# Kernel optimization log

Hardware: AMD Instinct MI355X
Metric: run time of the kernel (lower is better)

Reference implementation:

```python
import jax, jax.numpy as jnp
import numpy as np

B, S, D = 8, 2048, 1024
NEG = 1e9  # mask penalty used by the original module


def setup_inputs() -> dict:
    key = jax.random.key(0)
    kq, kk, km = jax.random.split(key, 3)
    q = jax.random.normal(kq, (B, S, D), dtype=jnp.float32)
    k = jax.random.normal(kk, (B, S, D), dtype=jnp.float32)
    # True = valid token, False = padding (module uses logical_not(mask) as pad)
    mask = jax.random.randint(km, (B, S), 0, 2).astype(bool)
    # learnable scalar scale, initialized to 1 (use_scale=True)
    scale = jnp.ones((), dtype=jnp.float32)
    return {"q": q, "k": k, "mask": mask, "scale": scale}


def reference(q, k, mask, scale):
    # v = k (sources has 2 entries when mask is provided)
    scores = jnp.einsum("bqd,bkd->bqk", q, k) * scale          # [B,S,S]
    pad = jnp.logical_not(mask).astype(scores.dtype)[:, :, None]  # [B,S,1]
    pad = jnp.maximum(pad, jnp.swapaxes(pad, 1, 2))             # [B,S,S]
    seq = jnp.triu(jnp.ones((S, S), scores.dtype), k=1)[None]   # [1,S,S] causal
    attn_mask = jnp.maximum(pad, seq)
    scores = scores - NEG * attn_mask
    attn = jax.nn.softmax(scores, axis=-1)
    feat = jnp.einsum("bqk,bkd->bqd", attn, k)                  # [B,S,D]
    return feat
```

## Files before the change

kernel.cpp:

```cpp
#include <hip/hip_runtime.h>
#include <hip/hip_bf16.h>
#include <stdint.h>

#define S_ 2048
#define D_ 1024
#define B_ 8
#define KEXP 3072
#define NEGC 1e9f

typedef _Float16 f16;
typedef _Float16 f16x8 __attribute__((ext_vector_type(8)));
typedef float f32x4 __attribute__((ext_vector_type(4)));

#define DSR(dst, addr, off) \
  asm volatile("ds_read_b128 %0, %1 offset:%c2" : "=v"(dst) : "v"(addr), "i"(off))
#define WAITL(n) do { asm volatile("s_waitcnt lgkmcnt(%c0)" :: "i"(n) : "memory"); \
                      __builtin_amdgcn_sched_barrier(0); } while (0)
#define VMC(n) asm volatile("s_waitcnt vmcnt(%c0)" :: "i"(n) : "memory")
#define BAR() __builtin_amdgcn_s_barrier()

__global__ __launch_bounds__(256) void split_expand2(const float* __restrict__ qin,
                                                     const float* __restrict__ kin,
                                                     f16* __restrict__ qx,
                                                     f16* __restrict__ kx) {
  const int isB = blockIdx.y;
  const float* in = isB ? kin : qin;
  f16* out = isB ? kx : qx;
  size_t idx = (size_t)blockIdx.x * 256 + threadIdx.x;
  const float4* ip = (const float4*)(in + idx * 8);
  float4 a = ip[0], b = ip[1];
  float vv[8] = {a.x, a.y, a.z, a.w, b.x, b.y, b.z, b.w};
  union { f16 h[24]; uint4 u[3]; } o;
#pragma unroll
  for (int t = 0; t < 8; ++t) {
    float v = vv[t] * 64.0f;
    f16 h = (f16)v;
    float r = v - (float)h;
    f16 l = (f16)r;
    o.h[3 * t + 0] = h;
    o.h[3 * t + 1] = isB ? h : l;
    o.h[3 * t + 2] = isB ? l : h;
  }
  uint4* op = (uint4*)(out + idx * 24);
  op[0] = o.u[0]; op[1] = o.u[1]; op[2] = o.u[2];
}

__global__ __launch_bounds__(256) void transpose_cast(const float* __restrict__ k,
                                                      f16* __restrict__ khT) {
  __shared__ f16 tile[64][65];
  int j0 = blockIdx.x * 64, d0 = blockIdx.y * 64;
  size_t bz = blockIdx.z;
  const float* kb = k + bz * (size_t)S_ * D_;
  f16* ob = khT + bz * (size_t)D_ * S_;
#pragma unroll
  for (int i = 0; i < 16; ++i) {
    int e = threadIdx.x + i * 256;
    int r = e >> 6, c = e & 63;
    tile[c][r] = (f16)kb[(size_t)(j0 + r) * D_ + d0 + c];
  }
  __syncthreads();
#pragma unroll
  for (int i = 0; i < 16; ++i) {
    int e = threadIdx.x + i * 256;
    int r = e >> 6, c = e & 63;
    ob[(size_t)(d0 + r) * S_ + j0 + c] = tile[r][c];
  }
}

template <int KA, int NN, int BN, int PIPE>
__global__ __launch_bounds__(512, PIPE ? 1 : 2) void gemm8p(const f16* __restrict__ A,
                                                            const f16* __restrict__ Bm,
                                                            float* __restrict__ C,
                                                            const float* scale_ptr,
                                                            float factor) {
  constexpr int NFQ = BN / 128;
  constexpr int GB = NFQ;
  constexpr int NB = 2 * NFQ;
  constexpr int VP3 = 2 + GB;
  constexpr int VP7 = 2 + 2 * GB;
  constexpr int VPR = 4 + 2 * GB;
  constexpr int NI = KA / 128;
  __shared__ f16 AS[2][256 * 64];
  __shared__ f16 BS[2][BN * 64];

  const int tid = threadIdx.x;
  const int lane = tid & 63, wave = tid >> 6;
  const int wm = wave >> 2, wn = wave & 3;
  const int fr = lane & 15, kq = lane >> 4;

  int lin = blockIdx.x + gridDim.x * blockIdx.y;
  int ntot = gridDim.x * gridDim.y;
  int nid = (lin & 7) * (ntot >> 3) + (lin >> 3);
  int bz = nid >> 6, rem = nid & 63;
  int bx = rem & 7, by = rem >> 3;

  const f16* Ab = A + (size_t)bz * S_ * KA + (size_t)bx * 256 * KA;
  const f16* Bb = Bm + (size_t)bz * NN * KA + (size_t)by * BN * KA;

  const int T0 = fr * 128 + (((0 + kq) ^ (fr & 7)) << 4);
  const int T1 = fr * 128 + (((4 + kq) ^ (fr & 7)) << 4);
  uint32_t asbase = (uint32_t)(uintptr_t)(__attribute__((address_space(3))) f16*)&AS[0][0];
  uint32_t bsbase = (uint32_t)(uintptr_t)(__attribute__((address_space(3))) f16*)&BS[0][0];
  uint32_t aA[2][2], aB[2][2];
#pragma unroll
  for (int b = 0; b < 2; ++b) {
    aA[b][0] = asbase + b * 32768 + wm * 8192 + T0;
    aA[b][1] = asbase + b * 32768 + wm * 8192 + T1;
    aB[b][0] = bsbase + b * (BN * 128) + wn * (BN * 16) + T0;
    aB[b][1] = bsbase + b * (BN * 128) + wn * (BN * 16) + T1;
  }

  const int srl = tid >> 3;
  const int sgc = ((((tid * 16) & 127) ^ (((tid >> 3) & 7) << 4)) >> 1);

  auto stgA = [&](int buf, int unit, int kt) {
#pragma unroll
    for (int i = 0; i < 2; ++i) {
      const f16* src = Ab + (size_t)(unit * 128 + i * 64 + srl) * KA + kt * 64 + sgc;
      __builtin_amdgcn_global_load_lds(
          (const __attribute__((address_space(1))) void*)src,
          (__attribute__((address_space(3))) void*)&AS[buf][unit * 8192 + i * 4096 + wave * 512],
          16, 0, 0);
    }
  };
  auto stgB = [&](int buf, int unit, int kt) {
#pragma unroll
    for (int i = 0; i < GB; ++i) {
      const f16* src = Bb + (size_t)(unit * (BN / 2) + i * 64 + srl) * KA + kt * 64 + sgc;
      __builtin_amdgcn_global_load_lds(
          (const __attribute__((address_space(1))) void*)src,
          (__attribute__((address_space(3))) void*)&BS[buf][unit * (BN * 32) + i * 4096 + wave * 512],
          16, 0, 0);
    }
  };

  f32x4 acc[2][2][4][2];
#pragma unroll
  for (int mh = 0; mh < 2; ++mh)
#pragma unroll
    for (int nh = 0; nh < 2; ++nh)
#pragma unroll
      for (int m = 0; m < 4; ++m)
#pragma unroll
        for (int n = 0; n < NFQ; ++n)
#pragma unroll
          for (int r = 0; r < 4; ++r) acc[mh][nh][m][n][r] = 0.0f;

#define ISS_A(DST, UB, MH) do {                  \
    DSR(DST[0], aA[UB][0], (MH)*16384 + 0);      \
    DSR(DST[1], aA[UB][0], (MH)*16384 + 2048);   \
    DSR(DST[2], aA[UB][0], (MH)*16384 + 4096);   \
    DSR(DST[3], aA[UB][0], (MH)*16384 + 6144);   \
    DSR(DST[4], aA[UB][1], (MH)*16384 + 0);      \
    DSR(DST[5], aA[UB][1], (MH)*16384 + 2048);   \
    DSR(DST[6], aA[UB][1], (MH)*16384 + 4096);   \
    DSR(DST[7], aA[UB][1], (MH)*16384 + 6144);   \
  } while (0)

#define ISS_B(DST, UB, NH) do {                       \
    DSR(DST[0], aB[UB][0], (NH) * (BN * 64) + 0);     \
    DSR(DST[1], aB[UB][1], (NH) * (BN * 64) + 0);     \
    if constexpr (NFQ == 2) {                         \
      DSR(DST[2], aB[UB][0], (NH) * (BN * 64) + 2048);\
      DSR(DST[3], aB[UB][1], (NH) * (BN * 64) + 2048);\
    }                                                 \
  } while (0)

#define MMX(MH, NH, AF, BF) do {                                                          \
    __builtin_amdgcn_s_setprio(1);                                                        \
    _Pragma("unroll")                                                                     \
    for (int m = 0; m < 4; ++m) {                                                         \
      acc[MH][NH][m][0] = __builtin_amdgcn_mfma_f32_16x16x32_f16(AF[m], BF[0], acc[MH][NH][m][0], 0, 0, 0);     \
      acc[MH][NH][m][0] = __builtin_amdgcn_mfma_f32_16x16x32_f16(AF[4 + m], BF[1], acc[MH][NH][m][0], 0, 0, 0); \
      if constexpr (NFQ == 2) {                                                           \
        acc[MH][NH][m][1] = __builtin_amdgcn_mfma_f32_16x16x32_f16(AF[m], BF[2], acc[MH][NH][m][1], 0, 0, 0);     \
        acc[MH][NH][m][1] = __builtin_amdgcn_mfma_f32_16x16x32_f16(AF[4 + m], BF[3], acc[MH][NH][m][1], 0, 0, 0); \
      }                                                                                   \
    }                                                                                     \
    __builtin_amdgcn_s_setprio(0);                                                        \
  } while (0)

  if constexpr (!PIPE) {
    stgA(0, 0, 0); stgA(0, 1, 0); stgB(0, 0, 0); stgB(0, 1, 0);
    stgA(1, 0, 1);
    VMC(0); BAR();

#pragma unroll 1
    for (int I = 0; I < NI; ++I) {
      const int v = 2 * I + 1, u2 = 2 * I + 2, v2 = 2 * I + 3;
      const bool st = (I + 1 < NI);
      f16x8 af[8], bf[4];
      ISS_A(af, 0, 0); ISS_B(bf, 0, 0); stgA(1, 1, v);
      WAITL(0); MMX(0, 0, af, bf); BAR();
      ISS_B(bf, 0, 1); stgB(1, 0, v); stgB(1, 1, v);
      WAITL(0); MMX(0, 1, af, bf); BAR();
      ISS_A(af, 0, 1); if (st) stgA(0, 0, u2);
      WAITL(0); MMX(1, 1, af, bf); BAR();
      ISS_B(bf, 0, 0); if (st) stgA(0, 1, u2);
      WAITL(0); MMX(1, 0, af, bf);
      if (st) { VMC(4); } else { VMC(0); }
      BAR();
      ISS_A(af, 1, 0); ISS_B(bf, 1, 0); if (st) stgB(0, 1, u2);
      WAITL(0); MMX(0, 0, af, bf); BAR();
      ISS_B(bf, 1, 1); if (st) stgB(0, 0, u2);
      WAITL(0); MMX(0, 1, af, bf); BAR();
      ISS_A(af, 1, 1); if (st) stgA(1, 0, v2);
      WAITL(0); MMX(1, 1, af, bf); BAR();
      ISS_B(bf, 1, 0);
      WAITL(0); MMX(1, 0, af, bf);
      if (st) { VMC(2); }
      BAR();
    }
  } else {
    f16x8 afX[8], afY[8], bfP[4], bfQ[4];
    stgA(0, 0, 0); stgA(0, 1, 0); stgB(0, 0, 0); stgB(0, 1, 0);
    stgA(1, 0, 1); stgA(1, 1, 1); stgB(1, 0, 1); stgB(1, 1, 1);
    VMC(VPR); BAR();
    ISS_A(afX, 0, 0); ISS_B(bfP, 0, 0);

#pragma unroll 1
    for (int I = 0; I < NI; ++I) {
      const int u2 = 2 * I + 2, v2 = 2 * I + 3;
      const bool st = (I + 1 < NI);
      ISS_B(bfQ, 0, 1);
      WAITL(NB); MMX(0, 0, afX, bfP); BAR();
      ISS_A(afY, 0, 1);
      if (st) stgA(0, 0, u2);
      WAITL(8); MMX(0, 1, afX, bfQ); BAR();
      ISS_B(bfP, 0, 0);
      if (st) stgB(0, 1, u2);
      WAITL(NB); MMX(1, 1, afY, bfQ);
      if (st) { VMC(VP3); } else { VMC(0); }
      BAR();
      ISS_A(afX, 1, 0); ISS_B(bfQ, 1, 0);
      if (st) stgA(0, 1, u2);
      WAITL(8 + NB); MMX(1, 0, afY, bfP); BAR();
      ISS_B(bfP, 1, 1);
      if (st) stgB(0, 0, u2);
      WAITL(NB); MMX(0, 0, afX, bfQ); BAR();
      ISS_A(afY, 1, 1);
      if (st) { stgA(1, 0, v2); stgB(1, 0, v2); }
      WAITL(8); MMX(0, 1, afX, bfP); BAR();
      if (st) stgB(1, 1, v2);
      WAITL(0); MMX(1, 1, afY, bfP);
      if (st) { VMC(VP7); }
      BAR();
      if (st) {
        ISS_A(afX, 0, 0); ISS_B(bfP, 0, 0);
        stgA(1, 1, v2);
        WAITL(8 + NB);
      } else {
        WAITL(0);
      }
      MMX(1, 0, afY, bfQ); BAR();
    }
  }
#undef ISS_A
#undef ISS_B
#undef MMX

  float scl = factor;
  if (scale_ptr != nullptr) scl = factor * scale_ptr[0];
  float* Cb = C + (size_t)bz * S_ * NN;
  const int r0 = bx * 256 + wm * 64 + kq * 4;
  const int c0 = by * BN + wn * (BN / 8) + fr;
#pragma unroll
  for (int mh = 0; mh < 2; ++mh)
#pragma unroll
    for (int nh = 0; nh < 2; ++nh)
#pragma unroll
      for (int m = 0; m < 4; ++m)
#pragma unroll
        for (int n = 0; n < NFQ; ++n)
#pragma unroll
          for (int r = 0; r < 4; ++r)
            Cb[(size_t)(r0 + mh * 128 + m * 16 + r) * NN + c0 + nh * (BN / 2) + n * 16] =
                acc[mh][nh][m][n][r] * scl;
}

__device__ __forceinline__ float block_reduce_max(float v, float* red, int tid) {
#pragma unroll
  for (int o = 32; o > 0; o >>= 1) v = fmaxf(v, __shfl_xor(v, o, 64));
  __syncthreads();
  if ((tid & 63) == 0) red[tid >> 6] = v;
  __syncthreads();
  return fmaxf(fmaxf(red[0], red[1]), fmaxf(red[2], red[3]));
}
__device__ __forceinline__ float block_reduce_sum(float v, float* red, int tid) {
#pragma unroll
  for (int o = 32; o > 0; o >>= 1) v += __shfl_xor(v, o, 64);
  __syncthreads();
  if ((tid & 63) == 0) red[4 + (tid >> 6)] = v;
  __syncthreads();
  return (red[4] + red[5]) + (red[6] + red[7]);
}

__global__ __launch_bounds__(256) void softmax_rows(const float* __restrict__ scores,
                                                    const int* __restrict__ mask,
                                                    const float* __restrict__ qg,
                                                    const float* __restrict__ kg,
                                                    const float* __restrict__ scale_ptr,
                                                    f16* __restrict__ P, int b0) {
  __shared__ float red[8];
  const int q = blockIdx.x, bl = blockIdx.y, bg = b0 + bl;
  const int tid = threadIdx.x;
  const float* srow = scores + ((size_t)bl * S_ + q) * S_;
  f16* prow = P + ((size_t)bl * S_ + q) * S_;
  const int j0 = tid * 8;
  float4 s0v = *(const float4*)(srow + j0);
  float4 s1v = *(const float4*)(srow + j0 + 4);
  float sv[8] = {s0v.x, s0v.y, s0v.z, s0v.w, s1v.x, s1v.y, s1v.z, s1v.w};

  if (mask[bg * S_ + q] == 0) {
    float vv[8];
    float lm = -3.4e38f;
#pragma unroll
    for (int i = 0; i < 8; ++i) {
      vv[i] = sv[i] - NEGC;
      lm = fmaxf(lm, vv[i]);
    }
    float g0 = block_reduce_max(lm, red, tid);
    float lm2 = -3.4e38f;
#pragma unroll 1
    for (int i = 0; i < 8; ++i) {
      float s = sv[i];
      float t = s * (1.0f / 64.0f);
      float rn = rintf(t);
      float dist = (0.5f - fabsf(t - rn)) * 64.0f;
      float v = vv[i];
      if (dist < 1e-3f && v >= g0 - 64.5f) {
        const float* qr = qg + ((size_t)bg * S_ + q) * D_;
        const float* kr = kg + ((size_t)bg * S_ + j0 + i) * D_;
        double acc = 0.0;
        for (int t2 = 0; t2 < D_; ++t2) acc += (double)qr[t2] * (double)kr[t2];
        v = (float)acc * scale_ptr[0] - NEGC;
      }
      vv[i] = v;
      lm2 = fmaxf(lm2, v);
    }
    float gf = block_reduce_max(lm2, red, tid);
    float local = 0.0f;
#pragma unroll
    for (int i = 0; i < 8; ++i) local += (vv[i] == gf) ? 1.0f : 0.0f;
    float cnt = block_reduce_sum(local, red, tid);
    f16 inv = (f16)(1.0f / cnt);
    union { f16 h[8]; uint4 u; } ow;
#pragma unroll
    for (int i = 0; i < 8; ++i) ow.h[i] = (vv[i] == gf) ? inv : (f16)0.0f;
    *(uint4*)(prow + j0) = ow.u;
    return;
  }

  int4 m0 = *(const int4*)(mask + (size_t)bg * S_ + j0);
  int4 m1 = *(const int4*)(mask + (size_t)bg * S_ + j0 + 4);
  int mk[8] = {m0.x, m0.y, m0.z, m0.w, m1.x, m1.y, m1.z, m1.w};
  int fl[8];
  float lm = -3.4e38f;
#pragma unroll
  for (int i = 0; i < 8; ++i) {
    fl[i] = (j0 + i <= q) && (mk[i] != 0);
    if (fl[i]) lm = fmaxf(lm, sv[i]);
  }
  float m = block_reduce_max(lm, red, tid);
  float ls = 0.0f;
#pragma unroll
  for (int i = 0; i < 8; ++i) {
    float e = fl[i] ? expf(sv[i] - m) : 0.0f;
    sv[i] = e; ls += e;
  }
  float sum = block_reduce_sum(ls, red, tid);
  float inv = 1.0f / sum;
  union { f16 h[8]; uint4 u; } ow;
#pragma unroll
  for (int i = 0; i < 8; ++i) ow.h[i] = (f16)(sv[i] * inv);
  *(uint4*)(prow + j0) = ow.u;
}

extern "C" void kernel_launch(void* const* d_in, const int* in_sizes, int n_in,
                              void* d_out, int out_size, void* d_ws, size_t ws_size,
                              hipStream_t stream) {
  (void)in_sizes; (void)n_in; (void)out_size;
  const float* q = (const float*)d_in[0];
  const float* k = (const float*)d_in[1];
  const int* mask = (const int*)d_in[2];
  const float* scale = (const float*)d_in[3];
  float* out = (float*)d_out;

  const size_t per_qx = (size_t)S_ * KEXP * 2;
  const size_t per_khT = (size_t)D_ * S_ * 2;
  const size_t per_sc = (size_t)S_ * S_ * 4;
  const size_t per_batch = 2 * per_qx + per_khT + per_sc;

  int nb = (int)(ws_size / per_batch);
  if (nb > 4) nb = 4;
  if (nb < 1) nb = 1;

  char* w = (char*)d_ws;
  f16* qx = (f16*)w;
  f16* kx = (f16*)(w + (size_t)nb * per_qx);
  f16* khT = (f16*)(w + (size_t)nb * per_qx * 2);
  float* sc = (float*)(w + (size_t)nb * (per_qx * 2 + per_khT));
  f16* P = qx;

  for (int b0 = 0; b0 < B_; b0 += nb) {
    int cb = (B_ - b0 < nb) ? (B_ - b0) : nb;
    const float* qb = q + (size_t)b0 * S_ * D_;
    const float* kb = k + (size_t)b0 * S_ * D_;

    int blocks0 = cb * ((S_ * D_ / 8) / 256);
    split_expand2<<<dim3(blocks0, 2), dim3(256), 0, stream>>>(qb, kb, qx, kx);
    transpose_cast<<<dim3(S_ / 64, D_ / 64, cb), dim3(256), 0, stream>>>(kb, khT);

    gemm8p<KEXP, S_, 256, 0><<<dim3(64, cb), dim3(512), 0, stream>>>(
        qx, kx, sc, scale, 0.000244140625f);

    softmax_rows<<<dim3(S_, cb), dim3(256), 0, stream>>>(sc, mask, q, k, scale, P, b0);

    gemm8p<S_, D_, 128, 1><<<dim3(64, cb), dim3(512), 0, stream>>>(
        P, khT, out + (size_t)b0 * S_ * D_, nullptr, 1.0f);
  }
}
```

Measured before the change: 428.6 us.

## Split GEMM template and give PV GEMM a triple-buffered LDS pipeline

Separates the QK and PV GEMMs into dedicated kernels. The PV GEMM moves to a 3-stage shared-memory ring with 64-wide K steps, issuing global-to-LDS loads two stages ahead and using one barrier per step instead of eight barriers per 128-K iteration. The aim is to cut synchronisation and overlap memory loads with MFMA work. In exchange it uses 1.5x the LDS (144KB) and has coarser waits, which could limit latency hiding within a step.

```diff
diff --git a/kernel.cpp b/kernel.cpp
--- a/kernel.cpp
+++ b/kernel.cpp
@@ -67,18 +67,14 @@
   }
 }
 
-template <int KA, int NN, int BN, int PIPE>
-__global__ __launch_bounds__(512, PIPE ? 1 : 2) void gemm8p(const f16* __restrict__ A,
-                                                            const f16* __restrict__ Bm,
-                                                            float* __restrict__ C,
-                                                            const float* scale_ptr,
-                                                            float factor) {
+template <int KA, int NN, int BN>
+__global__ __launch_bounds__(512, 2) void gemmQK(const f16* __restrict__ A,
+                                                 const f16* __restrict__ Bm,
+                                                 float* __restrict__ C,
+                                                 const float* scale_ptr,
+                                                 float factor) {
   constexpr int NFQ = BN / 128;
   constexpr int GB = NFQ;
-  constexpr int NB = 2 * NFQ;
-  constexpr int VP3 = 2 + GB;
-  constexpr int VP7 = 2 + 2 * GB;
-  constexpr int VPR = 4 + 2 * GB;
   constexpr int NI = KA / 128;
   __shared__ f16 AS[2][256 * 64];
   __shared__ f16 BS[2][BN * 64];
@@ -160,10 +156,8 @@
 #define ISS_B(DST, UB, NH) do {                       \
     DSR(DST[0], aB[UB][0], (NH) * (BN * 64) + 0);     \
     DSR(DST[1], aB[UB][1], (NH) * (BN * 64) + 0);     \
-    if constexpr (NFQ == 2) {                         \
-      DSR(DST[2], aB[UB][0], (NH) * (BN * 64) + 2048);\
-      DSR(DST[3], aB[UB][1], (NH) * (BN * 64) + 2048);\
-    }                                                 \
+    DSR(DST[2], aB[UB][0], (NH) * (BN * 64) + 2048);  \
+    DSR(DST[3], aB[UB][1], (NH) * (BN * 64) + 2048);  \
   } while (0)
 
 #define MMX(MH, NH, AF, BF) do {                                                          \
@@ -172,88 +166,41 @@
     for (int m = 0; m < 4; ++m) {                                                         \
       acc[MH][NH][m][0] = __builtin_amdgcn_mfma_f32_16x16x32_f16(AF[m], BF[0], acc[MH][NH][m][0], 0, 0, 0);     \
       acc[MH][NH][m][0] = __builtin_amdgcn_mfma_f32_16x16x32_f16(AF[4 + m], BF[1], acc[MH][NH][m][0], 0, 0, 0); \
-      if constexpr (NFQ == 2) {                                                           \
-        acc[MH][NH][m][1] = __builtin_amdgcn_mfma_f32_16x16x32_f16(AF[m], BF[2], acc[MH][NH][m][1], 0, 0, 0);     \
-        acc[MH][NH][m][1] = __builtin_amdgcn_mfma_f32_16x16x32_f16(AF[4 + m], BF[3], acc[MH][NH][m][1], 0, 0, 0); \
-      }                                                                                   \
+      acc[MH][NH][m][1] = __builtin_amdgcn_mfma_f32_16x16x32_f16(AF[m], BF[2], acc[MH][NH][m][1], 0, 0, 0);     \
+      acc[MH][NH][m][1] = __builtin_amdgcn_mfma_f32_16x16x32_f16(AF[4 + m], BF[3], acc[MH][NH][m][1], 0, 0, 0); \
     }                                                                                     \
     __builtin_amdgcn_s_setprio(0);                                                        \
   } while (0)
 
-  if constexpr (!PIPE) {
-    stgA(0, 0, 0); stgA(0, 1, 0); stgB(0, 0, 0); stgB(0, 1, 0);
-    stgA(1, 0, 1);
-    VMC(0); BAR();
+  stgA(0, 0, 0); stgA(0, 1, 0); stgB(0, 0, 0); stgB(0, 1, 0);
+  stgA(1, 0, 1);
+  VMC(0); BAR();
 
 #pragma unroll 1
-    for (int I = 0; I < NI; ++I) {
-      const int v = 2 * I + 1, u2 = 2 * I + 2, v2 = 2 * I + 3;
-      const bool st = (I + 1 < NI);
-      f16x8 af[8], bf[4];
-      ISS_A(af, 0, 0); ISS_B(bf, 0, 0); stgA(1, 1, v);
-      WAITL(0); MMX(0, 0, af, bf); BAR();
-      ISS_B(bf, 0, 1); stgB(1, 0, v); stgB(1, 1, v);
-      WAITL(0); MMX(0, 1, af, bf); BAR();
-      ISS_A(af, 0, 1); if (st) stgA(0, 0, u2);
-      WAITL(0); MMX(1, 1, af, bf); BAR();
-      ISS_B(bf, 0, 0); if (st) stgA(0, 1, u2);
-      WAITL(0); MMX(1, 0, af, bf);
-      if (st) { VMC(4); } else { VMC(0); }
-      BAR();
-      ISS_A(af, 1, 0); ISS_B(bf, 1, 0); if (st) stgB(0, 1, u2);
-      WAITL(0); MMX(0, 0, af, bf); BAR();
-      ISS_B(bf, 1, 1); if (st) stgB(0, 0, u2);
-      WAITL(0); MMX(0, 1, af, bf); BAR();
-      ISS_A(af, 1, 1); if (st) stgA(1, 0, v2);
-      WAITL(0); MMX(1, 1, af, bf); BAR();
-      ISS_B(bf, 1, 0);
-      WAITL(0); MMX(1, 0, af, bf);
-      if (st) { VMC(2); }
-      BAR();
-    }
-  } else {
-    f16x8 afX[8], afY[8], bfP[4], bfQ[4];
-    stgA(0, 0, 0); stgA(0, 1, 0); stgB(0, 0, 0); stgB(0, 1, 0);
-    stgA(1, 0, 1); stgA(1, 1, 1); stgB(1, 0, 1); stgB(1, 1, 1);
-    VMC(VPR); BAR();
-    ISS_A(afX, 0, 0); ISS_B(bfP, 0, 0);
-
-#pragma unroll 1
-    for (int I = 0; I < NI; ++I) {
-      const int u2 = 2 * I + 2, v2 = 2 * I + 3;
-      const bool st = (I + 1 < NI);
-      ISS_B(bfQ, 0, 1);
-      WAITL(NB); MMX(0, 0, afX, bfP); BAR();
-      ISS_A(afY, 0, 1);
-      if (st) stgA(0, 0, u2);
-      WAITL(8); MMX(0, 1, afX, bfQ); BAR();
-      ISS_B(bfP, 0, 0);
-      if (st) stgB(0, 1, u2);
-      WAITL(NB); MMX(1, 1, afY, bfQ);
-      if (st) { VMC(VP3); } else { VMC(0); }
-      BAR();
-      ISS_A(afX, 1, 0); ISS_B(bfQ, 1, 0);
-      if (st) stgA(0, 1, u2);
-      WAITL(8 + NB); MMX(1, 0, afY, bfP); BAR();
-      ISS_B(bfP, 1, 1);
-      if (st) stgB(0, 0, u2);
-      WAITL(NB); MMX(0, 0, afX, bfQ); BAR();
-      ISS_A(afY, 1, 1);
-      if (st) { stgA(1, 0, v2); stgB(1, 0, v2); }
-      WAITL(8); MMX(0, 1, afX, bfP); BAR();
-      if (st) stgB(1, 1, v2);
-      WAITL(0); MMX(1, 1, afY, bfP);
-      if (st) { VMC(VP7); }
-      BAR();
-      if (st) {
-        ISS_A(afX, 0, 0); ISS_B(bfP, 0, 0);
-        stgA(1, 1, v2);
-        WAITL(8 + NB);
-      } else {
-        WAITL(0);
-      }
-      MMX(1, 0, afY, bfQ); BAR();
-    }
+  for (int I = 0; I < NI; ++I) {
+    const int v = 2 * I + 1, u2 = 2 * I + 2, v2 = 2 * I + 3;
+    const bool st = (I + 1 < NI);
+    f16x8 af[8], bf[4];
+    ISS_A(af, 0, 0); ISS_B(bf, 0, 0); stgA(1, 1, v);
+    WAITL(0); MMX(0, 0, af, bf); BAR();
+    ISS_B(bf, 0, 1); stgB(1, 0, v); stgB(1, 1, v);
+    WAITL(0); MMX(0, 1, af, bf); BAR();
+    ISS_A(af, 0, 1); if (st) stgA(0, 0, u2);
+    WAITL(0); MMX(1, 1, af, bf); BAR();
+    ISS_B(bf, 0, 0); if (st) stgA(0, 1, u2);
+    WAITL(0); MMX(1, 0, af, bf);
+    if (st) { VMC(4); } else { VMC(0); }
+    BAR();
+    ISS_A(af, 1, 0); ISS_B(bf, 1, 0); if (st) stgB(0, 1, u2);
+    WAITL(0); MMX(0, 0, af, bf); BAR();
+    ISS_B(bf, 1, 1); if (st) stgB(0, 0, u2);
+    WAITL(0); MMX(0, 1, af, bf); BAR();
+    ISS_A(af, 1, 1); if (st) stgA(1, 0, v2);
+    WAITL(0); MMX(1, 1, af, bf); BAR();
+    ISS_B(bf, 1, 0);
+    WAITL(0); MMX(1, 0, af, bf);
+    if (st) { VMC(2); }
+    BAR();
   }
 #undef ISS_A
 #undef ISS_B
@@ -276,6 +223,141 @@
           for (int r = 0; r < 4; ++r)
             Cb[(size_t)(r0 + mh * 128 + m * 16 + r) * NN + c0 + nh * (BN / 2) + n * 16] =
                 acc[mh][nh][m][n][r] * scl;
+}
+
+template <int KA, int NN>
+__global__ __launch_bounds__(512, 1) void gemmPV(const f16* __restrict__ A,
+                                                 const f16* __restrict__ Bm,
+                                                 float* __restrict__ C,
+                                                 float factor) {
+  constexpr int BN = 128;
+  constexpr int NT = KA / 64;
+  __shared__ f16 AS[3][256 * 64];
+  __shared__ f16 BS[3][BN * 64];
+
+  const int tid = threadIdx.x;
+  const int lane = tid & 63, wave = tid >> 6;
+  const int wm = wave >> 2, wn = wave & 3;
+  const int fr = lane & 15, kq = lane >> 4;
+
+  int lin = blockIdx.x + gridDim.x * blockIdx.y;
+  int ntot = gridDim.x * gridDim.y;
+  int nid = (lin & 7) * (ntot >> 3) + (lin >> 3);
+  int bz = nid >> 6, rem = nid & 63;
+  int bx = rem & 7, by = rem >> 3;
+
+  const f16* Ab = A + (size_t)bz * S_ * KA + (size_t)bx * 256 * KA;
+  const f16* Bb = Bm + (size_t)bz * NN * KA + (size_t)by * BN * KA;
+
+  const int T0 = fr * 128 + (((0 + kq) ^ (fr & 7)) << 4);
+  const int T1 = fr * 128 + (((4 + kq) ^ (fr & 7)) << 4);
+  uint32_t asbase = (uint32_t)(uintptr_t)(__attribute__((address_space(3))) f16*)&AS[0][0];
+  uint32_t bsbase = (uint32_t)(uintptr_t)(__attribute__((address_space(3))) f16*)&BS[0][0];
+  uint32_t aA[3][2], aB[3][2];
+#pragma unroll
+  for (int s = 0; s < 3; ++s) {
+    aA[s][0] = asbase + s * 32768 + wm * 8192 + T0;
+    aA[s][1] = asbase + s * 32768 + wm * 8192 + T1;
+    aB[s][0] = bsbase + s * 16384 + wn * (BN * 16) + T0;
+    aB[s][1] = bsbase + s * 16384 + wn * (BN * 16) + T1;
+  }
+
+  const int srl = tid >> 3;
+  const int sgc = ((((tid * 16) & 127) ^ (((tid >> 3) & 7) << 4)) >> 1);
+
+  auto stgA = [&](int slot, int unit, int kt) {
+#pragma unroll
+    for (int i = 0; i < 2; ++i) {
+      const f16* src = Ab + (size_t)(unit * 128 + i * 64 + srl) * KA + kt * 64 + sgc;
+      __builtin_amdgcn_global_load_lds(
+          (const __attribute__((address_space(1))) void*)src,
+          (__attribute__((address_space(3))) void*)&AS[slot][unit * 8192 + i * 4096 + wave * 512],
+          16, 0, 0);
+    }
+  };
+  auto stgB = [&](int slot, int unit, int kt) {
+    const f16* src = Bb + (size_t)(unit * (BN / 2) + srl) * KA + kt * 64 + sgc;
+    __builtin_amdgcn_global_load_lds(
+        (const __attribute__((address_space(1))) void*)src,
+        (__attribute__((address_space(3))) void*)&BS[slot][unit * (BN * 32) + wave * 512],
+        16, 0, 0);
+  };
+
+  f32x4 acc[2][2][4];
+#pragma unroll
+  for (int mh = 0; mh < 2; ++mh)
+#pragma unroll
+    for (int nh = 0; nh < 2; ++nh)
+#pragma unroll
+      for (int m = 0; m < 4; ++m)
+#pragma unroll
+        for (int r = 0; r < 4; ++r) acc[mh][nh][m][r] = 0.0f;
+
+#define PISS_A(DST, S, MH) do {                  \
+    DSR(DST[0], aA[S][0], (MH)*16384 + 0);       \
+    DSR(DST[1], aA[S][0], (MH)*16384 + 2048);    \
+    DSR(DST[2], aA[S][0], (MH)*16384 + 4096);    \
+    DSR(DST[3], aA[S][0], (MH)*16384 + 6144);    \
+    DSR(DST[4], aA[S][1], (MH)*16384 + 0);       \
+    DSR(DST[5], aA[S][1], (MH)*16384 + 2048);    \
+    DSR(DST[6], aA[S][1], (MH)*16384 + 4096);    \
+    DSR(DST[7], aA[S][1], (MH)*16384 + 6144);    \
+  } while (0)
+
+#define PISS_B(DST, S, NH) do {                       \
+    DSR(DST[0], aB[S][0], (NH) * (BN * 64) + 0);      \
+    DSR(DST[1], aB[S][1], (NH) * (BN * 64) + 0);      \
+  } while (0)
+
+#define PMM(MH, NH, AF, BF) do {                                                          \
+    __builtin_amdgcn_s_setprio(1);                                                        \
+    _Pragma("unroll")                                                                     \
+    for (int m = 0; m < 4; ++m) {                                                         \
+      acc[MH][NH][m] = __builtin_amdgcn_mfma_f32_16x16x32_f16(AF[m], BF[0], acc[MH][NH][m], 0, 0, 0);     \
+      acc[MH][NH][m] = __builtin_amdgcn_mfma_f32_16x16x32_f16(AF[4 + m], BF[1], acc[MH][NH][m], 0, 0, 0); \
+    }                                                                                     \
+    __builtin_amdgcn_s_setprio(0);                                                        \
+  } while (0)
+
+  stgA(0, 0, 0); stgA(0, 1, 0); stgB(0, 0, 0); stgB(0, 1, 0);
+  stgA(1, 0, 1); stgA(1, 1, 1); stgB(1, 0, 1); stgB(1, 1, 1);
+  VMC(6); BAR();
+
+#pragma unroll 1
+  for (int t = 0; t < NT; ++t) {
+    const int s = t % 3, sn = (t + 2) % 3;
+    const bool st2 = (t + 2 < NT);
+    f16x8 afX[8], afY[8], bfP[2], bfQ[2];
+    PISS_A(afX, s, 0); PISS_B(bfP, s, 0); PISS_B(bfQ, s, 1);
+    if (st2) { stgA(sn, 0, t + 2); stgA(sn, 1, t + 2); stgB(sn, 0, t + 2); stgB(sn, 1, t + 2); }
+    WAITL(2);
+    PMM(0, 0, afX, bfP);
+    WAITL(0);
+    PMM(0, 1, afX, bfQ);
+    PISS_A(afY, s, 1);
+    WAITL(0);
+    PMM(1, 1, afY, bfQ);
+    PMM(1, 0, afY, bfP);
+    if (st2) { VMC(6); } else { VMC(0); }
+    BAR();
+  }
+#undef PISS_A
+#undef PISS_B
+#undef PMM
+
+  float* Cb = C + (size_t)bz * S_ * NN;
+  const int r0 = bx * 256 + wm * 64 + kq * 4;
+  const int c0 = by * BN + wn * (BN / 8) + fr;
+#pragma unroll
+  for (int mh = 0; mh < 2; ++mh)
+#pragma unroll
+    for (int nh = 0; nh < 2; ++nh)
+#pragma unroll
+      for (int m = 0; m < 4; ++m)
+#pragma unroll
+        for (int r = 0; r < 4; ++r)
+          Cb[(size_t)(r0 + mh * 128 + m * 16 + r) * NN + c0 + nh * (BN / 2)] =
+              acc[mh][nh][m][r] * factor;
 }
 
 __device__ __forceinline__ float block_reduce_max(float v, float* red, int tid) {
@@ -411,12 +493,12 @@
     split_expand2<<<dim3(blocks0, 2), dim3(256), 0, stream>>>(qb, kb, qx, kx);
     transpose_cast<<<dim3(S_ / 64, D_ / 64, cb), dim3(256), 0, stream>>>(kb, khT);
 
-    gemm8p<KEXP, S_, 256, 0><<<dim3(64, cb), dim3(512), 0, stream>>>(
+    gemmQK<KEXP, S_, 256><<<dim3(64, cb), dim3(512), 0, stream>>>(
         qx, kx, sc, scale, 0.000244140625f);
 
     softmax_rows<<<dim3(S_, cb), dim3(256), 0, stream>>>(sc, mask, q, k, scale, P, b0);
 
-    gemm8p<S_, D_, 128, 1><<<dim3(64, cb), dim3(512), 0, stream>>>(
-        P, khT, out + (size_t)b0 * S_ * D_, nullptr, 1.0f);
-  }
-}
+    gemmPV<S_, D_><<<dim3(64, cb), dim3(512), 0, stream>>>(
+        P, khT, out + (size_t)b0 * S_ * D_, 1.0f);
+  }
+}
```

Result: no change. 436.3 us (+1.8%).
